# Performance work log

Measured on AMD Instinct MI355X. Metric: run time of the kernel, lower is better.

Reference implementation:

```python
import jax, jax.numpy as jnp
import numpy as np

STRIDES = [8, 16, 32, 64, 128]
FEATS = [128, 64, 32, 16, 8]
LEVEL_SIZES = [f * f for f in FEATS]
A_TOTAL = sum(LEVEL_SIZES)  # 21824
TOPK = 9
NUM_FG = 80          # config.num_classes - 1
ALPHA, GAMMA = 0.25, 2.0   # focal loss
JS_W = 0.1           # config.js_weight
B, M, IMG = 16, 32, 1024
EPS = 1e-6


def make_anchors():
    out = []
    for s, f in zip(STRIDES, FEATS):
        c = (np.arange(f, dtype=np.float32) + 0.5) * s
        cy, cx = np.meshgrid(c, c, indexing='ij')
        cx, cy = cx.reshape(-1), cy.reshape(-1)
        half = 4.0 * s
        out.append(np.stack([cx - half, cy - half, cx + half, cy + half], 1))
    return jnp.asarray(np.concatenate(out, 0), jnp.float32)


def pairwise_iou(a, g):
    # a: [A,4], g: [M,4] -> [A,M]
    tl = jnp.maximum(a[:, None, :2], g[None, :, :2])
    br = jnp.minimum(a[:, None, 2:], g[None, :, 2:])
    wh = jnp.clip(br - tl, 0.0)
    inter = wh[..., 0] * wh[..., 1]
    area_a = (a[:, 2] - a[:, 0]) * (a[:, 3] - a[:, 1])
    area_g = (g[:, 2] - g[:, 0]) * (g[:, 3] - g[:, 1])
    return inter / jnp.clip(area_a[:, None] + area_g[None, :] - inter, EPS)


def encode(gt, an):
    aw = an[:, 2] - an[:, 0]; ah = an[:, 3] - an[:, 1]
    ax = (an[:, 0] + an[:, 2]) * 0.5; ay = (an[:, 1] + an[:, 3]) * 0.5
    gw = jnp.clip(gt[:, 2] - gt[:, 0], EPS); gh = jnp.clip(gt[:, 3] - gt[:, 1], EPS)
    gx = (gt[:, 0] + gt[:, 2]) * 0.5; gy = (gt[:, 1] + gt[:, 3]) * 0.5
    return jnp.stack([(gx - ax) / aw, (gy - ay) / ah,
                      jnp.log(gw / aw), jnp.log(gh / ah)], 1)


def decode(delta, an):
    aw = an[:, 2] - an[:, 0]; ah = an[:, 3] - an[:, 1]
    ax = (an[:, 0] + an[:, 2]) * 0.5; ay = (an[:, 1] + an[:, 3]) * 0.5
    cx = ax + delta[:, 0] * aw; cy = ay + delta[:, 1] * ah
    w = jnp.exp(jnp.clip(delta[:, 2], -4.0, 4.0)) * aw
    h = jnp.exp(jnp.clip(delta[:, 3], -4.0, 4.0)) * ah
    return jnp.stack([cx - 0.5 * w, cy - 0.5 * h, cx + 0.5 * w, cy + 0.5 * h], 1)


def giou(b1, b2):
    tl = jnp.maximum(b1[:, :2], b2[:, :2]); br = jnp.minimum(b1[:, 2:], b2[:, 2:])
    wh = jnp.clip(br - tl, 0.0)
    inter = wh[:, 0] * wh[:, 1]
    a1 = (b1[:, 2] - b1[:, 0]) * (b1[:, 3] - b1[:, 1])
    a2 = (b2[:, 2] - b2[:, 0]) * (b2[:, 3] - b2[:, 1])
    union = jnp.clip(a1 + a2 - inter, EPS)
    iou = inter / union
    etl = jnp.minimum(b1[:, :2], b2[:, :2]); ebr = jnp.maximum(b1[:, 2:], b2[:, 2:])
    ewh = jnp.clip(ebr - etl, 0.0)
    enc = jnp.clip(ewh[:, 0] * ewh[:, 1], EPS)
    return iou - (enc - union) / enc


def assign_one(anchors, gts, glab):
    # ATSS assignment for one image. anchors [A,4], gts [M,4], glab [M]
    A = anchors.shape[0]; Mg = gts.shape[0]
    valid_gt = glab > 0
    ac = (anchors[:, :2] + anchors[:, 2:]) * 0.5           # [A,2]
    gc = (gts[:, :2] + gts[:, 2:]) * 0.5                   # [M,2]
    dist = jnp.linalg.norm(ac[:, None, :] - gc[None, :, :], axis=-1)  # [A,M]
    iou = pairwise_iou(anchors, gts)                       # [A,M]
    cand = []
    start = 0
    for n in LEVEL_SIZES:  # fixed small level loop
        d = dist[start:start + n].T                        # [M,n]
        k = min(TOPK, n)
        _, idx = jax.lax.top_k(-d, k)                      # [M,k]
        cand.append(idx + start)
        start += n
    cand = jnp.concatenate(cand, axis=1)                   # [M,K]
    iou_t = iou.T                                          # [M,A]
    cand_iou = jnp.take_along_axis(iou_t, cand, axis=1)    # [M,K]
    thr = cand_iou.mean(1) + jnp.std(cand_iou, axis=1, ddof=1)
    ccx = ac[:, 0][cand]; ccy = ac[:, 1][cand]
    l = ccx - gts[:, 0:1]; t = ccy - gts[:, 1:2]
    r = gts[:, 2:3] - ccx; b = gts[:, 3:4] - ccy
    inside = jnp.minimum(jnp.minimum(l, r), jnp.minimum(t, b)) > 0.01
    pos_cand = (cand_iou >= thr[:, None]) & inside & valid_gt[:, None]
    rows = jnp.arange(Mg)[:, None]
    pos_mask = jnp.zeros((Mg, A), jnp.int32).at[rows, cand].add(pos_cand.astype(jnp.int32)) > 0
    iou_masked = jnp.where(pos_mask, iou_t, -1.0)          # [M,A]
    best_gt = jnp.argmax(iou_masked, axis=0)               # [A]
    best_iou = jnp.max(iou_masked, axis=0)
    fg = best_iou > -0.5
    labels = jnp.where(fg, glab[best_gt].astype(jnp.int32), 0)
    bbox_tgt = encode(gts[best_gt], anchors)               # [A,4]
    return labels, bbox_tgt


def _forward(pred_cls, pred_reg, pred_ctn, anchors, gt_boxes):
    labels, bbox_t = jax.vmap(assign_one, in_axes=(None, 0, 0))(
        anchors, gt_boxes[..., :4], gt_boxes[..., 4])
    labels = labels.reshape(-1)              # [B*A]
    bbox_t = bbox_t.reshape(-1, 4)
    anc = jnp.tile(anchors, (B, 1))          # [B*A,4]
    fg = (labels > 0).astype(pred_cls.dtype)
    valid = (labels >= 0).astype(pred_cls.dtype)

    # focal loss on sigmoided logits
    p = jax.nn.sigmoid(pred_cls.reshape(-1, NUM_FG))
    onehot = (jnp.arange(NUM_FG)[None, :] == (labels - 1)[:, None]) & (labels > 0)[:, None]
    pos = -ALPHA * (1.0 - p) ** GAMMA * jnp.log(jnp.clip(p, 1e-12))
    neg = -(1.0 - ALPHA) * p ** GAMMA * jnp.log(jnp.clip(1.0 - p, 1e-12))
    loss_cls = (jnp.where(onehot, pos, neg).sum(-1) * valid).sum()

    # GIoU loss on decoded boxes
    pr = pred_reg.reshape(-1, 8)
    pbox = decode(pr[:, :4], anc)
    tbox = decode(bbox_t, anc)
    loss_reg = ((1.0 - giou(pbox, tbox)) * fg).sum()

    # centerness BCE
    acx = (anc[:, 0] + anc[:, 2]) * 0.5; acy = (anc[:, 1] + anc[:, 3]) * 0.5
    l = jnp.clip(acx - tbox[:, 0], EPS); r = jnp.clip(tbox[:, 2] - acx, EPS)
    t = jnp.clip(acy - tbox[:, 1], EPS); b = jnp.clip(tbox[:, 3] - acy, EPS)
    ctn = jnp.sqrt(jnp.clip(jnp.minimum(l, r) / jnp.maximum(l, r)
                            * jnp.minimum(t, b) / jnp.maximum(t, b), EPS, 1.0))
    logits = pred_ctn.reshape(-1)
    bce = jnp.clip(logits, 0.0) - logits * ctn + jnp.log1p(jnp.exp(-jnp.abs(logits)))
    loss_ctn = (bce * fg).sum()

    # Gaussian JS divergence: pred N(mu, exp(lstd)) vs target N(bbox_t, 1)
    mu = pr[:, :4]; lstd = pr[:, 4:]
    var = jnp.exp(2.0 * lstd)
    d2 = (mu - bbox_t) ** 2
    kl_pt = -lstd + 0.5 * (var + d2) - 0.5
    kl_tp = lstd + (1.0 + d2) / (2.0 * var) - 0.5
    loss_jsd = (0.5 * (kl_pt + kl_tp).sum(-1) * fg).sum() * JS_W

    ln = 0.9 * 100.0 + 0.1 * jnp.maximum(fg.sum(), 1.0)
    return jnp.stack([loss_cls, loss_reg, loss_ctn, loss_jsd]) / ln


def setup_inputs():
    key = jax.random.key(0)
    k1, k2, k3, k4, k5, k6, k7, k8 = jax.random.split(key, 8)
    pred_cls = jax.random.normal(k1, (B, A_TOTAL, NUM_FG), jnp.float32)
    pred_reg = 0.1 * jax.random.normal(k2, (B, A_TOTAL, 8), jnp.float32)
    pred_ctn = jax.random.normal(k3, (B, A_TOTAL), jnp.float32)
    anchors = make_anchors()
    x1 = jax.random.uniform(k4, (B, M)) * (IMG - 256)
    y1 = jax.random.uniform(k5, (B, M)) * (IMG - 256)
    wh = 32.0 + jax.random.uniform(k6, (B, M, 2)) * 192.0
    lab = jax.random.randint(k7, (B, M), 1, NUM_FG + 1).astype(jnp.float32)
    nvalid = jax.random.randint(k8, (B, 1), 5, M + 1)
    lab = jnp.where(jnp.arange(M)[None, :] < nvalid, lab, 0.0)
    gt_boxes = jnp.stack([x1, y1, x1 + wh[..., 0], y1 + wh[..., 1], lab], axis=-1)
    im_info = jnp.tile(jnp.array([IMG, IMG, 1.0, IMG, IMG, float(M)], jnp.float32), (B, 1))
    return {"pred_cls": pred_cls, "pred_reg": pred_reg, "pred_ctn": pred_ctn,
            "anchors": anchors, "gt_boxes": gt_boxes, "im_info": im_info}


def reference(pred_cls, pred_reg, pred_ctn, anchors, gt_boxes, im_info):
    return _forward(pred_cls, pred_reg, pred_ctn, anchors, gt_boxes)
```

## Files before the change

kernel.cpp:

```cpp
#include <hip/hip_runtime.h>
#include <math.h>

#define B_      16
#define M_      32
#define A_TOT   21824
#define NROWS   (B_*A_TOT)
#define NUM_FG_ 80
#define EPSF    1e-6f
#define NB0     1364
#define NB1     4096
#define NCAND   45

__device__ __forceinline__ float waveReduceSum(float v) {
    for (int o = 32; o > 0; o >>= 1) v += __shfl_down(v, o, 64);
    return v;
}
__device__ __forceinline__ unsigned long long waveReduceMinU64(unsigned long long v) {
    for (int o = 32; o > 0; o >>= 1) {
        unsigned long long other = __shfl_down(v, o, 64);
        v = other < v ? other : v;
    }
    return v;
}

__global__ __launch_bounds__(64) void k_assign(
    const float* __restrict__ anchors,
    const float* __restrict__ gtb,
    unsigned long long* __restrict__ keys)
{
    const int   lvl_base[5] = {0, 16384, 20480, 21504, 21760};
    const int   lvl_f[5]    = {128, 64, 32, 16, 8};
    const float lvl_s[5]    = {8.f, 16.f, 32.f, 64.f, 128.f};
    int bg = blockIdx.x;
    int b = bg >> 5, g = bg & 31;
    const float* gt = gtb + (b * M_ + g) * 5;
    float g0 = gt[0], g1 = gt[1], g2 = gt[2], g3 = gt[3];
    bool valid = gt[4] > 0.f;
    float gcx = (g0 + g2) * 0.5f, gcy = (g1 + g3) * 0.5f;
    int lane = threadIdx.x;
    __shared__ int cand[NCAND];

    for (int l = 0; l < 5; ++l) {
        int f = lvl_f[l], base = lvl_base[l];
        float s = lvl_s[l];
        int ixn = (int)floorf(gcx / s); ixn = min(max(ixn, 0), f - 1);
        int iyn = (int)floorf(gcy / s); iyn = min(max(iyn, 0), f - 1);
        int ix0 = min(max(ixn - 3, 0), f - 7);
        int iy0 = min(max(iyn - 3, 0), f - 7);
        unsigned long long key = ~0ULL;
        if (lane < 49) {
            int ix = ix0 + lane % 7, iy = iy0 + lane / 7;
            int a = base + iy * f + ix;
            float4 an = ((const float4*)anchors)[a];
            float acx = (an.x + an.z) * 0.5f, acy = (an.y + an.w) * 0.5f;
            float dx = acx - gcx, dy = acy - gcy;
            float dist = sqrtf(dx * dx + dy * dy);
            key = ((unsigned long long)__float_as_uint(dist) << 32) | (unsigned)a;
        }
        for (int j = 0; j < 9; ++j) {
            unsigned long long m = waveReduceMinU64(key);
            m = __shfl(m, 0, 64);
            if (key == m) key = ~0ULL;
            if (lane == 0) cand[l * 9 + j] = (int)(m & 0xffffffffu);
        }
    }
    __syncthreads();

    float iou = 0.f; bool inside = false; int a = 0;
    if (lane < NCAND) {
        a = cand[lane];
        float4 an = ((const float4*)anchors)[a];
        float tlx = fmaxf(an.x, g0), tly = fmaxf(an.y, g1);
        float brx = fminf(an.z, g2), bry = fminf(an.w, g3);
        float w = fmaxf(brx - tlx, 0.f), h = fmaxf(bry - tly, 0.f);
        float inter = w * h;
        float aa = (an.z - an.x) * (an.w - an.y);
        float ag = (g2 - g0) * (g3 - g1);
        iou = inter / fmaxf(aa + ag - inter, EPSF);
        float ccx = (an.x + an.z) * 0.5f, ccy = (an.y + an.w) * 0.5f;
        float li = ccx - g0, ti = ccy - g1, ri = g2 - ccx, bi = g3 - ccy;
        inside = fminf(fminf(li, ri), fminf(ti, bi)) > 0.01f;
    }
    float s = waveReduceSum(lane < NCAND ? iou : 0.f);
    float mean = __shfl(s, 0, 64) * (1.f / 45.f);
    float d = (lane < NCAND) ? (iou - mean) : 0.f;
    float ss = waveReduceSum(d * d);
    float thr = mean + sqrtf(__shfl(ss, 0, 64) * (1.f / 44.f));
    if (lane < NCAND && valid && inside && iou >= thr) {
        unsigned long long key =
            ((unsigned long long)__float_as_uint(iou) << 32) | (unsigned)(31 - g);
        atomicMax(&keys[(size_t)b * A_TOT + a], key);
    }
}

__global__ __launch_bounds__(256) void k_row(
    const float* __restrict__ pred_reg,
    const float* __restrict__ pred_ctn,
    const float* __restrict__ anchors,
    const float* __restrict__ gtb,
    const unsigned long long* __restrict__ keys,
    double* __restrict__ part0)
{
    int t = blockIdx.x * 256 + threadIdx.x;
    float reg = 0.f, ctn = 0.f, jsd = 0.f, fgc = 0.f;
    if (t < NROWS) {
        unsigned long long key = keys[t];
        if (key) {
            fgc = 1.f;
            int b = t / A_TOT;
            int a = t - b * A_TOT;
            int g = 31 - (int)(key & 0xffffffffu);
            const float* gt = gtb + (b * M_ + g) * 5;
            float g0 = gt[0], g1 = gt[1], g2 = gt[2], g3 = gt[3];
            float4 an = ((const float4*)anchors)[a];
            float aw = an.z - an.x, ah = an.w - an.y;
            float ax = (an.x + an.z) * 0.5f, ay = (an.y + an.w) * 0.5f;
            float gw = fmaxf(g2 - g0, EPSF), gh = fmaxf(g3 - g1, EPSF);
            float gx = (g0 + g2) * 0.5f, gy = (g1 + g3) * 0.5f;
            float e0 = (gx - ax) / aw, e1 = (gy - ay) / ah;
            float e2 = __logf(gw / aw), e3 = __logf(gh / ah);
            float tw = __expf(fminf(fmaxf(e2, -4.f), 4.f)) * aw;
            float th = __expf(fminf(fmaxf(e3, -4.f), 4.f)) * ah;
            float tcx = ax + e0 * aw, tcy = ay + e1 * ah;
            float tb0 = tcx - 0.5f * tw, tb1 = tcy - 0.5f * th;
            float tb2 = tcx + 0.5f * tw, tb3 = tcy + 0.5f * th;
            const float* pr = pred_reg + (size_t)t * 8;
            float p0 = pr[0], p1 = pr[1], p2 = pr[2], p3 = pr[3];
            float l0 = pr[4], l1 = pr[5], l2 = pr[6], l3 = pr[7];
            float pw = __expf(fminf(fmaxf(p2, -4.f), 4.f)) * aw;
            float ph = __expf(fminf(fmaxf(p3, -4.f), 4.f)) * ah;
            float pcx = ax + p0 * aw, pcy = ay + p1 * ah;
            float pb0 = pcx - 0.5f * pw, pb1 = pcy - 0.5f * ph;
            float pb2 = pcx + 0.5f * pw, pb3 = pcy + 0.5f * ph;
            float tlx = fmaxf(pb0, tb0), tly = fmaxf(pb1, tb1);
            float brx = fminf(pb2, tb2), bry = fminf(pb3, tb3);
            float iw = fmaxf(brx - tlx, 0.f), ih = fmaxf(bry - tly, 0.f);
            float inter = iw * ih;
            float a1 = (pb2 - pb0) * (pb3 - pb1);
            float a2 = (tb2 - tb0) * (tb3 - tb1);
            float uni = fmaxf(a1 + a2 - inter, EPSF);
            float iou = inter / uni;
            float ex0 = fminf(pb0, tb0), ey0 = fminf(pb1, tb1);
            float ex1 = fmaxf(pb2, tb2), ey1 = fmaxf(pb3, tb3);
            float ew = fmaxf(ex1 - ex0, 0.f), eh = fmaxf(ey1 - ey0, 0.f);
            float enc = fmaxf(ew * eh, EPSF);
            reg = 1.f - (iou - (enc - uni) / enc);
            float cl = fmaxf(ax - tb0, EPSF), cr = fmaxf(tb2 - ax, EPSF);
            float ct = fmaxf(ay - tb1, EPSF), cb = fmaxf(tb3 - ay, EPSF);
            float ratio = fminf(cl, cr) / fmaxf(cl, cr) * (fminf(ct, cb) / fmaxf(ct, cb));
            float cstar = sqrtf(fminf(fmaxf(ratio, EPSF), 1.f));
            float z = pred_ctn[t];
            ctn = fmaxf(z, 0.f) - z * cstar + log1pf(__expf(-fabsf(z)));
            float mu[4] = {p0, p1, p2, p3}, ls[4] = {l0, l1, l2, l3};
            float ee[4] = {e0, e1, e2, e3};
            float ksum = 0.f;
#pragma unroll
            for (int i = 0; i < 4; ++i) {
                float var = __expf(2.f * ls[i]);
                float d2 = (mu[i] - ee[i]) * (mu[i] - ee[i]);
                float kl_pt = -ls[i] + 0.5f * (var + d2) - 0.5f;
                float kl_tp = ls[i] + (1.f + d2) / (2.f * var) - 0.5f;
                ksum += kl_pt + kl_tp;
            }
            jsd = 0.5f * ksum;
        }
    }
    float vr = waveReduceSum(reg), vc = waveReduceSum(ctn);
    float vj = waveReduceSum(jsd), vf = waveReduceSum(fgc);
    __shared__ float sbuf[4][4];
    int wid = threadIdx.x >> 6, lid = threadIdx.x & 63;
    if (lid == 0) { sbuf[wid][0] = vr; sbuf[wid][1] = vc; sbuf[wid][2] = vj; sbuf[wid][3] = vf; }
    __syncthreads();
    if (threadIdx.x == 0) {
        double r = 0, c = 0, j = 0, f = 0;
        for (int w = 0; w < 4; ++w) { r += sbuf[w][0]; c += sbuf[w][1]; j += sbuf[w][2]; f += sbuf[w][3]; }
        part0[blockIdx.x * 4 + 0] = r; part0[blockIdx.x * 4 + 1] = c;
        part0[blockIdx.x * 4 + 2] = j; part0[blockIdx.x * 4 + 3] = f;
    }
}

__global__ __launch_bounds__(256) void k_cls(
    const float4* __restrict__ cls4,
    const float* __restrict__ gtb,
    const unsigned long long* __restrict__ keys,
    double* __restrict__ part1)
{
    const int total4 = NROWS * (NUM_FG_ / 4);
    float acc = 0.f;
    for (int i = blockIdx.x * 256 + threadIdx.x; i < total4; i += gridDim.x * 256) {
        float4 v = cls4[i];
        int row = i / 20;
        int c0 = (i - row * 20) * 4;
        unsigned long long key = keys[row];
        int tgt = -1;
        if (key) {
            int b = row / A_TOT;
            int g = 31 - (int)(key & 0xffffffffu);
            tgt = (int)gtb[(b * M_ + g) * 5 + 4] - 1;
        }
        float xs[4] = {v.x, v.y, v.z, v.w};
#pragma unroll
        for (int j = 0; j < 4; ++j) {
            float x = xs[j];
            float p = 1.f / (1.f + __expf(-x));
            float loss;
            if (c0 + j == tgt)
                loss = -0.25f * (1.f - p) * (1.f - p) * __logf(fmaxf(p, 1e-12f));
            else
                loss = -0.75f * p * p * __logf(fmaxf(1.f - p, 1e-12f));
            acc += loss;
        }
    }
    acc = waveReduceSum(acc);
    __shared__ float sb[4];
    int wid = threadIdx.x >> 6, lid = threadIdx.x & 63;
    if (lid == 0) sb[wid] = acc;
    __syncthreads();
    if (threadIdx.x == 0)
        part1[blockIdx.x] = (double)sb[0] + sb[1] + sb[2] + sb[3];
}

__global__ __launch_bounds__(256) void k_final(
    const double* __restrict__ part0,
    const double* __restrict__ part1,
    float* __restrict__ out)
{
    double cls = 0, reg = 0, ctn = 0, jsd = 0, fgc = 0;
    for (int i = threadIdx.x; i < NB1; i += 256) cls += part1[i];
    for (int i = threadIdx.x; i < NB0; i += 256) {
        reg += part0[i * 4 + 0]; ctn += part0[i * 4 + 1];
        jsd += part0[i * 4 + 2]; fgc += part0[i * 4 + 3];
    }
    for (int o = 32; o > 0; o >>= 1) {
        cls += __shfl_down(cls, o, 64); reg += __shfl_down(reg, o, 64);
        ctn += __shfl_down(ctn, o, 64); jsd += __shfl_down(jsd, o, 64);
        fgc += __shfl_down(fgc, o, 64);
    }
    __shared__ double sb[5][4];
    int wid = threadIdx.x >> 6, lid = threadIdx.x & 63;
    if (lid == 0) { sb[0][wid] = cls; sb[1][wid] = reg; sb[2][wid] = ctn; sb[3][wid] = jsd; sb[4][wid] = fgc; }
    __syncthreads();
    if (threadIdx.x == 0) {
        double C = sb[0][0] + sb[0][1] + sb[0][2] + sb[0][3];
        double R = sb[1][0] + sb[1][1] + sb[1][2] + sb[1][3];
        double T = sb[2][0] + sb[2][1] + sb[2][2] + sb[2][3];
        double J = sb[3][0] + sb[3][1] + sb[3][2] + sb[3][3];
        double F = sb[4][0] + sb[4][1] + sb[4][2] + sb[4][3];
        double ln = 0.9 * 100.0 + 0.1 * fmax(F, 1.0);
        out[0] = (float)(C / ln);
        out[1] = (float)(R / ln);
        out[2] = (float)(T / ln);
        out[3] = (float)(0.1 * J / ln);
    }
}

extern "C" void kernel_launch(void* const* d_in, const int* in_sizes, int n_in,
                              void* d_out, int out_size, void* d_ws, size_t ws_size,
                              hipStream_t stream) {
    (void)in_sizes; (void)n_in; (void)out_size; (void)ws_size;
    const float* pred_cls = (const float*)d_in[0];
    const float* pred_reg = (const float*)d_in[1];
    const float* pred_ctn = (const float*)d_in[2];
    const float* anchors  = (const float*)d_in[3];
    const float* gtb      = (const float*)d_in[4];

    unsigned long long* keys = (unsigned long long*)d_ws;
    double* part0 = (double*)((char*)d_ws + (size_t)NROWS * 8);
    double* part1 = part0 + (size_t)NB0 * 4;

    hipMemsetAsync(keys, 0, (size_t)NROWS * 8, stream);
    k_assign<<<B_ * M_, 64, 0, stream>>>(anchors, gtb, keys);
    k_row   <<<NB0, 256, 0, stream>>>(pred_reg, pred_ctn, anchors, gtb, keys, part0);
    k_cls   <<<NB1, 256, 0, stream>>>((const float4*)pred_cls, gtb, keys, part1);
    k_final <<<1, 256, 0, stream>>>(part0, part1, (float*)d_out);
}
```

Measured before the change: 210.1 us.

## Fuse row and classification loss kernels; parallel rank-based top-k in assignment

Merges the per-row regression/centerness/JSD kernel into the classification focal-loss grid-stride kernel, so each foreground row's extra work runs in the thread that handles its first class chunk. This removes one launch and a second pass over keys. The assignment kernel replaces 45 sequential wave-min reductions with a parallel rank count over shared-memory keys, and computes anchor centres arithmetically instead of loading them. The cost is divergence inside the fused loop, since only some lanes do the heavy regression math. Grid size drops to 2048 blocks.

```diff
diff --git a/kernel.cpp b/kernel.cpp
--- a/kernel.cpp
+++ b/kernel.cpp
@@ -7,19 +7,11 @@
 #define NROWS   (B_*A_TOT)
 #define NUM_FG_ 80
 #define EPSF    1e-6f
-#define NB0     1364
-#define NB1     4096
 #define NCAND   45
+#define NBF     2048
 
 __device__ __forceinline__ float waveReduceSum(float v) {
     for (int o = 32; o > 0; o >>= 1) v += __shfl_down(v, o, 64);
-    return v;
-}
-__device__ __forceinline__ unsigned long long waveReduceMinU64(unsigned long long v) {
-    for (int o = 32; o > 0; o >>= 1) {
-        unsigned long long other = __shfl_down(v, o, 64);
-        v = other < v ? other : v;
-    }
     return v;
 }
 
@@ -38,30 +30,45 @@
     bool valid = gt[4] > 0.f;
     float gcx = (g0 + g2) * 0.5f, gcy = (g1 + g3) * 0.5f;
     int lane = threadIdx.x;
+
+    __shared__ unsigned long long kbuf[5 * 49];
     __shared__ int cand[NCAND];
 
-    for (int l = 0; l < 5; ++l) {
-        int f = lvl_f[l], base = lvl_base[l];
-        float s = lvl_s[l];
-        int ixn = (int)floorf(gcx / s); ixn = min(max(ixn, 0), f - 1);
-        int iyn = (int)floorf(gcy / s); iyn = min(max(iyn, 0), f - 1);
-        int ix0 = min(max(ixn - 3, 0), f - 7);
-        int iy0 = min(max(iyn - 3, 0), f - 7);
-        unsigned long long key = ~0ULL;
-        if (lane < 49) {
-            int ix = ix0 + lane % 7, iy = iy0 + lane / 7;
-            int a = base + iy * f + ix;
-            float4 an = ((const float4*)anchors)[a];
-            float acx = (an.x + an.z) * 0.5f, acy = (an.y + an.w) * 0.5f;
+    unsigned long long mykey[4];
+    int myanchor[4];
+#pragma unroll
+    for (int q = 0; q < 4; ++q) {
+        int cid = lane + 64 * q;
+        mykey[q] = ~0ULL;
+        if (cid < 245) {
+            int l = cid / 49, j = cid - l * 49;
+            int f = lvl_f[l];
+            float s = lvl_s[l];
+            int ixn = (int)floorf(gcx / s); ixn = min(max(ixn, 0), f - 1);
+            int iyn = (int)floorf(gcy / s); iyn = min(max(iyn, 0), f - 1);
+            int ix0 = min(max(ixn - 3, 0), f - 7);
+            int iy0 = min(max(iyn - 3, 0), f - 7);
+            int ix = ix0 + j % 7, iy = iy0 + j / 7;
+            int a = lvl_base[l] + iy * f + ix;
+            float acx = ((float)ix + 0.5f) * s;
+            float acy = ((float)iy + 0.5f) * s;
             float dx = acx - gcx, dy = acy - gcy;
             float dist = sqrtf(dx * dx + dy * dy);
-            key = ((unsigned long long)__float_as_uint(dist) << 32) | (unsigned)a;
-        }
-        for (int j = 0; j < 9; ++j) {
-            unsigned long long m = waveReduceMinU64(key);
-            m = __shfl(m, 0, 64);
-            if (key == m) key = ~0ULL;
-            if (lane == 0) cand[l * 9 + j] = (int)(m & 0xffffffffu);
+            mykey[q] = ((unsigned long long)__float_as_uint(dist) << 32) | (unsigned)a;
+            myanchor[q] = a;
+            kbuf[cid] = mykey[q];
+        }
+    }
+    __syncthreads();
+#pragma unroll
+    for (int q = 0; q < 4; ++q) {
+        int cid = lane + 64 * q;
+        if (cid < 245) {
+            int l = cid / 49;
+            const unsigned long long* kg = &kbuf[l * 49];
+            int cnt = 0;
+            for (int j = 0; j < 49; ++j) cnt += (kg[j] < mykey[q]);
+            if (cnt < 9) cand[l * 9 + cnt] = myanchor[q];
         }
     }
     __syncthreads();
@@ -93,26 +100,47 @@
     }
 }
 
-__global__ __launch_bounds__(256) void k_row(
+__global__ __launch_bounds__(256) void k_fused(
+    const float4* __restrict__ cls4,
     const float* __restrict__ pred_reg,
     const float* __restrict__ pred_ctn,
     const float* __restrict__ anchors,
     const float* __restrict__ gtb,
     const unsigned long long* __restrict__ keys,
-    double* __restrict__ part0)
+    double* __restrict__ part)
 {
-    int t = blockIdx.x * 256 + threadIdx.x;
-    float reg = 0.f, ctn = 0.f, jsd = 0.f, fgc = 0.f;
-    if (t < NROWS) {
-        unsigned long long key = keys[t];
+    const int total4 = NROWS * (NUM_FG_ / 4);
+    float accC = 0.f, accR = 0.f, accT = 0.f, accJ = 0.f, accF = 0.f;
+    for (int i = blockIdx.x * 256 + threadIdx.x; i < total4; i += NBF * 256) {
+        float4 v = cls4[i];
+        int row = i / 20;
+        int c0 = (i - row * 20) * 4;
+        unsigned long long key = keys[row];
+        int tgt = -1;
+        int b = row / A_TOT;
+        int g = 0;
         if (key) {
-            fgc = 1.f;
-            int b = t / A_TOT;
-            int a = t - b * A_TOT;
-            int g = 31 - (int)(key & 0xffffffffu);
+            g = 31 - (int)(key & 0xffffffffu);
+            tgt = (int)gtb[(b * M_ + g) * 5 + 4] - 1;
+        }
+        float xs[4] = {v.x, v.y, v.z, v.w};
+#pragma unroll
+        for (int j = 0; j < 4; ++j) {
+            float x = xs[j];
+            float p = 1.f / (1.f + __expf(-x));
+            float loss;
+            if (c0 + j == tgt)
+                loss = -0.25f * (1.f - p) * (1.f - p) * __logf(fmaxf(p, 1e-12f));
+            else
+                loss = -0.75f * p * p * __logf(fmaxf(1.f - p, 1e-12f));
+            accC += loss;
+        }
+        if (c0 == 0 && key) {
+            accF += 1.f;
+            int aidx = row - b * A_TOT;
             const float* gt = gtb + (b * M_ + g) * 5;
             float g0 = gt[0], g1 = gt[1], g2 = gt[2], g3 = gt[3];
-            float4 an = ((const float4*)anchors)[a];
+            float4 an = ((const float4*)anchors)[aidx];
             float aw = an.z - an.x, ah = an.w - an.y;
             float ax = (an.x + an.z) * 0.5f, ay = (an.y + an.w) * 0.5f;
             float gw = fmaxf(g2 - g0, EPSF), gh = fmaxf(g3 - g1, EPSF);
@@ -124,7 +152,7 @@
             float tcx = ax + e0 * aw, tcy = ay + e1 * ah;
             float tb0 = tcx - 0.5f * tw, tb1 = tcy - 0.5f * th;
             float tb2 = tcx + 0.5f * tw, tb3 = tcy + 0.5f * th;
-            const float* pr = pred_reg + (size_t)t * 8;
+            const float* pr = pred_reg + (size_t)row * 8;
             float p0 = pr[0], p1 = pr[1], p2 = pr[2], p3 = pr[3];
             float l0 = pr[4], l1 = pr[5], l2 = pr[6], l3 = pr[7];
             float pw = __expf(fminf(fmaxf(p2, -4.f), 4.f)) * aw;
@@ -144,113 +172,70 @@
             float ex1 = fmaxf(pb2, tb2), ey1 = fmaxf(pb3, tb3);
             float ew = fmaxf(ex1 - ex0, 0.f), eh = fmaxf(ey1 - ey0, 0.f);
             float enc = fmaxf(ew * eh, EPSF);
-            reg = 1.f - (iou - (enc - uni) / enc);
+            accR += 1.f - (iou - (enc - uni) / enc);
             float cl = fmaxf(ax - tb0, EPSF), cr = fmaxf(tb2 - ax, EPSF);
             float ct = fmaxf(ay - tb1, EPSF), cb = fmaxf(tb3 - ay, EPSF);
             float ratio = fminf(cl, cr) / fmaxf(cl, cr) * (fminf(ct, cb) / fmaxf(ct, cb));
             float cstar = sqrtf(fminf(fmaxf(ratio, EPSF), 1.f));
-            float z = pred_ctn[t];
-            ctn = fmaxf(z, 0.f) - z * cstar + log1pf(__expf(-fabsf(z)));
+            float z = pred_ctn[row];
+            accT += fmaxf(z, 0.f) - z * cstar + log1pf(__expf(-fabsf(z)));
             float mu[4] = {p0, p1, p2, p3}, ls[4] = {l0, l1, l2, l3};
             float ee[4] = {e0, e1, e2, e3};
             float ksum = 0.f;
 #pragma unroll
-            for (int i = 0; i < 4; ++i) {
-                float var = __expf(2.f * ls[i]);
-                float d2 = (mu[i] - ee[i]) * (mu[i] - ee[i]);
-                float kl_pt = -ls[i] + 0.5f * (var + d2) - 0.5f;
-                float kl_tp = ls[i] + (1.f + d2) / (2.f * var) - 0.5f;
-                ksum += kl_pt + kl_tp;
+            for (int k = 0; k < 4; ++k) {
+                float var = __expf(2.f * ls[k]);
+                float d2 = (mu[k] - ee[k]) * (mu[k] - ee[k]);
+                ksum += (-ls[k] + 0.5f * (var + d2) - 0.5f)
+                      + ( ls[k] + (1.f + d2) / (2.f * var) - 0.5f);
             }
-            jsd = 0.5f * ksum;
-        }
-    }
-    float vr = waveReduceSum(reg), vc = waveReduceSum(ctn);
-    float vj = waveReduceSum(jsd), vf = waveReduceSum(fgc);
-    __shared__ float sbuf[4][4];
+            accJ += 0.5f * ksum;
+        }
+    }
+    float vC = waveReduceSum(accC), vR = waveReduceSum(accR);
+    float vT = waveReduceSum(accT), vJ = waveReduceSum(accJ);
+    float vF = waveReduceSum(accF);
+    __shared__ float sb[4][5];
     int wid = threadIdx.x >> 6, lid = threadIdx.x & 63;
-    if (lid == 0) { sbuf[wid][0] = vr; sbuf[wid][1] = vc; sbuf[wid][2] = vj; sbuf[wid][3] = vf; }
+    if (lid == 0) { sb[wid][0]=vC; sb[wid][1]=vR; sb[wid][2]=vT; sb[wid][3]=vJ; sb[wid][4]=vF; }
     __syncthreads();
     if (threadIdx.x == 0) {
-        double r = 0, c = 0, j = 0, f = 0;
-        for (int w = 0; w < 4; ++w) { r += sbuf[w][0]; c += sbuf[w][1]; j += sbuf[w][2]; f += sbuf[w][3]; }
-        part0[blockIdx.x * 4 + 0] = r; part0[blockIdx.x * 4 + 1] = c;
-        part0[blockIdx.x * 4 + 2] = j; part0[blockIdx.x * 4 + 3] = f;
-    }
-}
-
-__global__ __launch_bounds__(256) void k_cls(
-    const float4* __restrict__ cls4,
-    const float* __restrict__ gtb,
-    const unsigned long long* __restrict__ keys,
-    double* __restrict__ part1)
-{
-    const int total4 = NROWS * (NUM_FG_ / 4);
-    float acc = 0.f;
-    for (int i = blockIdx.x * 256 + threadIdx.x; i < total4; i += gridDim.x * 256) {
-        float4 v = cls4[i];
-        int row = i / 20;
-        int c0 = (i - row * 20) * 4;
-        unsigned long long key = keys[row];
-        int tgt = -1;
-        if (key) {
-            int b = row / A_TOT;
-            int g = 31 - (int)(key & 0xffffffffu);
-            tgt = (int)gtb[(b * M_ + g) * 5 + 4] - 1;
-        }
-        float xs[4] = {v.x, v.y, v.z, v.w};
-#pragma unroll
-        for (int j = 0; j < 4; ++j) {
-            float x = xs[j];
-            float p = 1.f / (1.f + __expf(-x));
-            float loss;
-            if (c0 + j == tgt)
-                loss = -0.25f * (1.f - p) * (1.f - p) * __logf(fmaxf(p, 1e-12f));
-            else
-                loss = -0.75f * p * p * __logf(fmaxf(1.f - p, 1e-12f));
-            acc += loss;
-        }
-    }
-    acc = waveReduceSum(acc);
-    __shared__ float sb[4];
-    int wid = threadIdx.x >> 6, lid = threadIdx.x & 63;
-    if (lid == 0) sb[wid] = acc;
-    __syncthreads();
-    if (threadIdx.x == 0)
-        part1[blockIdx.x] = (double)sb[0] + sb[1] + sb[2] + sb[3];
+        double C=0,R=0,T=0,J=0,F=0;
+        for (int w = 0; w < 4; ++w) { C+=sb[w][0]; R+=sb[w][1]; T+=sb[w][2]; J+=sb[w][3]; F+=sb[w][4]; }
+        double* p = part + (size_t)blockIdx.x * 5;
+        p[0]=C; p[1]=R; p[2]=T; p[3]=J; p[4]=F;
+    }
 }
 
 __global__ __launch_bounds__(256) void k_final(
-    const double* __restrict__ part0,
-    const double* __restrict__ part1,
+    const double* __restrict__ part,
     float* __restrict__ out)
 {
-    double cls = 0, reg = 0, ctn = 0, jsd = 0, fgc = 0;
-    for (int i = threadIdx.x; i < NB1; i += 256) cls += part1[i];
-    for (int i = threadIdx.x; i < NB0; i += 256) {
-        reg += part0[i * 4 + 0]; ctn += part0[i * 4 + 1];
-        jsd += part0[i * 4 + 2]; fgc += part0[i * 4 + 3];
+    double C = 0, R = 0, T = 0, J = 0, F = 0;
+    for (int i = threadIdx.x; i < NBF; i += 256) {
+        const double* p = part + (size_t)i * 5;
+        C += p[0]; R += p[1]; T += p[2]; J += p[3]; F += p[4];
     }
     for (int o = 32; o > 0; o >>= 1) {
-        cls += __shfl_down(cls, o, 64); reg += __shfl_down(reg, o, 64);
-        ctn += __shfl_down(ctn, o, 64); jsd += __shfl_down(jsd, o, 64);
-        fgc += __shfl_down(fgc, o, 64);
+        C += __shfl_down(C, o, 64); R += __shfl_down(R, o, 64);
+        T += __shfl_down(T, o, 64); J += __shfl_down(J, o, 64);
+        F += __shfl_down(F, o, 64);
     }
     __shared__ double sb[5][4];
     int wid = threadIdx.x >> 6, lid = threadIdx.x & 63;
-    if (lid == 0) { sb[0][wid] = cls; sb[1][wid] = reg; sb[2][wid] = ctn; sb[3][wid] = jsd; sb[4][wid] = fgc; }
+    if (lid == 0) { sb[0][wid]=C; sb[1][wid]=R; sb[2][wid]=T; sb[3][wid]=J; sb[4][wid]=F; }
     __syncthreads();
     if (threadIdx.x == 0) {
-        double C = sb[0][0] + sb[0][1] + sb[0][2] + sb[0][3];
-        double R = sb[1][0] + sb[1][1] + sb[1][2] + sb[1][3];
-        double T = sb[2][0] + sb[2][1] + sb[2][2] + sb[2][3];
-        double J = sb[3][0] + sb[3][1] + sb[3][2] + sb[3][3];
-        double F = sb[4][0] + sb[4][1] + sb[4][2] + sb[4][3];
-        double ln = 0.9 * 100.0 + 0.1 * fmax(F, 1.0);
-        out[0] = (float)(C / ln);
-        out[1] = (float)(R / ln);
-        out[2] = (float)(T / ln);
-        out[3] = (float)(0.1 * J / ln);
+        double c = sb[0][0]+sb[0][1]+sb[0][2]+sb[0][3];
+        double r = sb[1][0]+sb[1][1]+sb[1][2]+sb[1][3];
+        double t = sb[2][0]+sb[2][1]+sb[2][2]+sb[2][3];
+        double j = sb[3][0]+sb[3][1]+sb[3][2]+sb[3][3];
+        double f = sb[4][0]+sb[4][1]+sb[4][2]+sb[4][3];
+        double ln = 0.9 * 100.0 + 0.1 * fmax(f, 1.0);
+        out[0] = (float)(c / ln);
+        out[1] = (float)(r / ln);
+        out[2] = (float)(t / ln);
+        out[3] = (float)(0.1 * j / ln);
     }
 }
 
@@ -265,12 +250,11 @@
     const float* gtb      = (const float*)d_in[4];
 
     unsigned long long* keys = (unsigned long long*)d_ws;
-    double* part0 = (double*)((char*)d_ws + (size_t)NROWS * 8);
-    double* part1 = part0 + (size_t)NB0 * 4;
+    double* part = (double*)((char*)d_ws + (size_t)NROWS * 8);
 
     hipMemsetAsync(keys, 0, (size_t)NROWS * 8, stream);
     k_assign<<<B_ * M_, 64, 0, stream>>>(anchors, gtb, keys);
-    k_row   <<<NB0, 256, 0, stream>>>(pred_reg, pred_ctn, anchors, gtb, keys, part0);
-    k_cls   <<<NB1, 256, 0, stream>>>((const float4*)pred_cls, gtb, keys, part1);
-    k_final <<<1, 256, 0, stream>>>(part0, part1, (float*)d_out);
-}
+    k_fused <<<NBF, 256, 0, stream>>>((const float4*)pred_cls, pred_reg, pred_ctn,
+                                      anchors, gtb, keys, part);
+    k_final <<<1, 256, 0, stream>>>(part, (float*)d_out);
+}
```

Measured after the change: 192.1 us. 1.09x faster.
